# Kernel optimization log

Hardware: AMD Instinct MI355X
Metric: run time of the kernel (lower is better)

Reference implementation:

```python
import jax, jax.numpy as jnp
import numpy as np

N, E = 100000, 600000
IN, H = 164, 128
NH = 4  # attention heads over embed_dim H//4 = 32


def layer_norm(x, g, b, eps=1e-5):
    m = x.mean(-1, keepdims=True)
    v = x.var(-1, keepdims=True)
    return (x - m) * jax.lax.rsqrt(v + eps) * g + b


def gcn_conv(x, W, b, src, dst, n):
    # PyG GCNConv: add self-loops, symmetric D^{-1/2}(A+I)D^{-1/2} normalization.
    deg = jnp.ones((n,), x.dtype).at[dst].add(1.0)  # degree of A+I on target nodes
    dinv = jax.lax.rsqrt(deg)
    xw = x @ W  # [n, out]
    msg = xw[src] * (dinv[src] * dinv[dst])[:, None]  # gather + edge-norm
    agg = jax.ops.segment_sum(msg, dst, num_segments=n)  # scatter-add
    agg = agg + xw * (dinv * dinv)[:, None]  # self-loop term
    return agg + b


def mha_seq1(x, Wq, bq, Wk, bk, Wv, bv, Wo, bo):
    # nn.MultiheadAttention with seq_len==1: softmax over a single key -> weights==1.
    dh = x.shape[-1] // NH
    q = (x @ Wq + bq).reshape(-1, NH, dh)
    k = (x @ Wk + bk).reshape(-1, NH, dh)
    v = (x @ Wv + bv).reshape(-1, NH, dh)
    scores = jnp.sum(q * k, -1, keepdims=True) / jnp.sqrt(jnp.float32(dh))  # [n,NH,1]
    attn = jax.nn.softmax(scores[..., None], axis=-1)[..., 0]  # all ones, kept for fidelity
    out = (attn * v).reshape(-1, NH * dh)
    return out @ Wo + bo


def setup_inputs() -> dict:
    key = jax.random.key(0)
    ks = jax.random.split(key, 16)

    def kaiming(k, i, o):
        return jax.random.normal(k, (i, o), jnp.float32) * (2.0 / i) ** 0.5

    Ha, Hb, Hc = H, H // 2, H // 4  # 128, 64, 32
    return {
        "x": jax.random.normal(ks[0], (N, IN), jnp.float32),
        "edge_index": jax.random.randint(ks[1], (2, E), 0, N),
        "Wi": kaiming(ks[2], IN, Ha), "bi": jnp.zeros((Ha,), jnp.float32),
        "g1": jnp.ones((Ha,), jnp.float32), "b1": jnp.zeros((Ha,), jnp.float32),
        "Wg1": kaiming(ks[3], Ha, Ha), "bg1": jnp.zeros((Ha,), jnp.float32),
        "Wg2": kaiming(ks[4], Ha, Hb), "bg2": jnp.zeros((Hb,), jnp.float32),
        "g2": jnp.ones((Hb,), jnp.float32), "b2": jnp.zeros((Hb,), jnp.float32),
        "Wg3": kaiming(ks[5], Hb, Hc), "bg3": jnp.zeros((Hc,), jnp.float32),
        "Wq": kaiming(ks[6], Hc, Hc), "bq": jnp.zeros((Hc,), jnp.float32),
        "Wk": kaiming(ks[7], Hc, Hc), "bk": jnp.zeros((Hc,), jnp.float32),
        "Wv": kaiming(ks[8], Hc, Hc), "bv": jnp.zeros((Hc,), jnp.float32),
        "Wo": kaiming(ks[9], Hc, Hc), "bo": jnp.zeros((Hc,), jnp.float32),
        "Wc1": kaiming(ks[10], Hc, H // 8), "bc1": jnp.zeros((H // 8,), jnp.float32),
        "Wc2": kaiming(ks[11], H // 8, 32), "bc2": jnp.zeros((32,), jnp.float32),
        "Wc3": kaiming(ks[12], 32, 1), "bc3": jnp.zeros((1,), jnp.float32),
    }


def reference(x, edge_index, Wi, bi, g1, b1, Wg1, bg1, Wg2, bg2, g2, b2,
              Wg3, bg3, Wq, bq, Wk, bk, Wv, bv, Wo, bo,
              Wc1, bc1, Wc2, bc2, Wc3, bc3):
    src, dst = edge_index[0], edge_index[1]
    n = x.shape[0]
    # dropout layers are identity in eval mode
    h = layer_norm(jax.nn.relu(x @ Wi + bi), g1, b1)
    h1 = jax.nn.relu(gcn_conv(h, Wg1, bg1, src, dst, n)) + h
    h2 = layer_norm(jax.nn.relu(gcn_conv(h1, Wg2, bg2, src, dst, n)), g2, b2)
    h3 = jax.nn.relu(gcn_conv(h2, Wg3, bg3, src, dst, n))
    h3 = mha_seq1(h3, Wq, bq, Wk, bk, Wv, bv, Wo, bo)
    h3 = jax.nn.relu(h3 @ Wc1 + bc1)
    h3 = jax.nn.relu(h3 @ Wc2 + bc2)
    return (h3 @ Wc3 + bc3)[:, 0]
```

## Files before the change

### kernel.cpp

```cpp
#include <hip/hip_runtime.h>


typedef __attribute__((ext_vector_type(8))) _Float16 f16x8;
typedef __attribute__((ext_vector_type(4))) _Float16 f16x4;
typedef __attribute__((ext_vector_type(4))) float f32x4;

template <int V> struct IC { static constexpr int value = V; };

#define GLOAD_LDS16(gp, lp)                                        \
  __builtin_amdgcn_global_load_lds(                                \
      (const __attribute__((address_space(1))) void*)(gp),         \
      (__attribute__((address_space(3))) void*)(lp), 16, 0, 0)

template <int NV>
static __device__ __forceinline__ void wait_vm() {
  asm volatile("s_waitcnt vmcnt(%0)" :: "n"(NV) : "memory");
}
static __device__ __forceinline__ void wait_lgkm0() {
  asm volatile("s_waitcnt lgkmcnt(0)" ::: "memory");
  __builtin_amdgcn_sched_barrier(0);
}

__global__ void k_count(const int* __restrict__ dst, int* __restrict__ counts, int e) {
  int i = blockIdx.x * blockDim.x + threadIdx.x;
  if (i < e) atomicAdd(&counts[dst[i]], 1);
}

__global__ __launch_bounds__(256) void k_scan_part(
    const int* __restrict__ counts, int* __restrict__ bsums, int n) {
  int tid = threadIdx.x;
  int i0 = blockIdx.x * 1024 + tid * 4;
  int s = 0;
#pragma unroll
  for (int k = 0; k < 4; k++) { int i = i0 + k; if (i < n) s += counts[i]; }
#pragma unroll
  for (int d = 1; d < 64; d <<= 1) s += __shfl_xor(s, d);
  __shared__ int wsum[4];
  int lane = tid & 63, w = tid >> 6;
  if (lane == 0) wsum[w] = s;
  __syncthreads();
  if (tid == 0) bsums[blockIdx.x] = wsum[0] + wsum[1] + wsum[2] + wsum[3];
}

__global__ __launch_bounds__(256) void k_scan_down(
    int* __restrict__ counts, const int* __restrict__ bsums,
    int* __restrict__ offsets, float* __restrict__ dinv, int n, int e, int nb) {
  int tid = threadIdx.x;
  int lane = tid & 63, w = tid >> 6;
  __shared__ int wsum[4], psum[4];
  int pv = (tid < nb && tid < blockIdx.x) ? bsums[tid] : 0;
#pragma unroll
  for (int d = 1; d < 64; d <<= 1) pv += __shfl_xor(pv, d);
  if (lane == 0) psum[w] = pv;
  __syncthreads();
  int blockpref = psum[0] + psum[1] + psum[2] + psum[3];

  int i0 = blockIdx.x * 1024 + tid * 4;
  int c[4]; int tsum = 0;
#pragma unroll
  for (int k = 0; k < 4; k++) { int i = i0 + k; c[k] = (i < n) ? counts[i] : 0; tsum += c[k]; }
  int v = tsum;
#pragma unroll
  for (int d = 1; d < 64; d <<= 1) { int t = __shfl_up(v, d); if (lane >= d) v += t; }
  if (lane == 63) wsum[w] = v;
  __syncthreads();
  int wadd = 0;
#pragma unroll
  for (int q = 0; q < 4; q++) if (q < w) wadd += wsum[q];
  int run = (v - tsum) + wadd + blockpref;
#pragma unroll
  for (int k = 0; k < 4; k++) {
    int i = i0 + k;
    if (i < n) {
      offsets[i] = run;
      dinv[i] = rsqrtf((float)(c[k] + 1));
      counts[i] = 0;
    }
    run += c[k];
  }
  if (blockIdx.x == 0 && tid == 0) offsets[n] = e;
}

__global__ void k_fill(const int* __restrict__ src, const int* __restrict__ dst,
                       const int* __restrict__ offsets, int* __restrict__ cursor,
                       const float* __restrict__ dinv, int2* __restrict__ csr, int e) {
  int i = blockIdx.x * blockDim.x + threadIdx.x;
  if (i >= e) return;
  int s = src[i], d = dst[i];
  int pos = atomicAdd(&cursor[d], 1);
  csr[offsets[d] + pos] = make_int2(s, __float_as_int(dinv[s] * dinv[d]));
}

__device__ __forceinline__ void pack_hi(const float* __restrict__ W,
                                        _Float16* __restrict__ dst,
                                        int K, int N, int u) {
  int lane = u & 63; int rest = u >> 6; int CT = N >> 4;
  int ct = rest % CT, ks = rest / CT;
  int gcol = ct * 16 + (lane & 15);
  int gk0 = ks * 32 + (lane >> 4) * 8;
  size_t o = (size_t)(ks * CT + ct) * 512 + lane * 8;
#pragma unroll
  for (int i = 0; i < 8; i++) {
    float v = (gk0 + i < K) ? W[(size_t)(gk0 + i) * N + gcol] : 0.0f;
    dst[o + i] = (_Float16)v;
  }
}

__global__ void k_setup(const float* __restrict__ Wi, const float* __restrict__ Wg1,
                        const float* __restrict__ Wg2, const float* __restrict__ Wg3,
                        _Float16* __restrict__ pWi, _Float16* __restrict__ pWg1,
                        _Float16* __restrict__ pWg2, _Float16* __restrict__ pWg3,
                        int* __restrict__ counts, float* __restrict__ zp, int n) {
  int b = blockIdx.x;
  if (b < 25) {
    int t = b * 256 + threadIdx.x;
    if (t < 3072) pack_hi(Wi, pWi, 164, 128, t);
    else if (t < 5120) pack_hi(Wg1, pWg1, 128, 128, t - 3072);
    else if (t < 6144) pack_hi(Wg2, pWg2, 128, 64, t - 5120);
    else if (t < 6400) pack_hi(Wg3, pWg3, 64, 32, t - 6144);
  } else {
    if (b == 25 && threadIdx.x < 64) zp[threadIdx.x] = 0.0f;
    int i = (b - 25) * 256 + threadIdx.x;
    if (i < n) counts[i] = 0;
  }
}

__global__ __launch_bounds__(512, 4) void k_gemm_in(
    const float* __restrict__ x, const _Float16* __restrict__ pB,
    const float* __restrict__ bias, const float* __restrict__ gamma,
    const float* __restrict__ beta, const float* __restrict__ zp,
    _Float16* __restrict__ out, int n) {
  constexpr int N = 128, CT = 8;
  __shared__ __align__(16) float sAi[8][3][512];
  int tid = threadIdx.x;
  int lane = tid & 63, w = tid >> 6;
  int rowbase = blockIdx.x * 128 + w * 16;
  const f16x8* Bf = (const f16x8*)pB;

  auto stage = [&](int ks, int buf) {
#pragma unroll
    for (int j = 0; j < 2; j++) {
      int r_ = j * 8 + (lane >> 3);
      int c_ = (lane & 7) ^ (lane >> 3);
      int rg = rowbase + r_;
      bool ok = (rg < n) && (ks < 5 || c_ == 0);
      const void* s = ok ? (const void*)(x + (size_t)rg * 164 + ks * 32 + c_ * 4)
                         : (const void*)zp;
      GLOAD_LDS16(s, &sAi[w][buf][j * 256]);
    }
  };

  f32x4 acc[CT];
#pragma unroll
  for (int c = 0; c < CT; c++) acc[c] = (f32x4)0.0f;

  int rr = lane & 15;
  int c0 = (lane >> 4) * 2;
  int s0 = c0 ^ (rr & 7);
  int s1 = (c0 + 1) ^ (rr & 7);

  f16x8 bfr[2][CT];
  stage(0, 0);
  stage(1, 1);
#pragma unroll
  for (int c = 0; c < CT; c++) bfr[0][c] = Bf[c * 64 + lane];

  auto step = [&](auto ksc, auto wnc) {
    constexpr int ks = decltype(ksc)::value;
    constexpr int WN = decltype(wnc)::value;
    if constexpr (ks + 1 < 6) {
#pragma unroll
      for (int c = 0; c < CT; c++)
        bfr[(ks + 1) & 1][c] = Bf[((ks + 1) * CT + c) * 64 + lane];
    }
    if constexpr (ks + 2 < 6) stage(ks + 2, (ks + 2) % 3);
    wait_vm<WN>();
    const float* bp = &sAi[w][ks % 3][0];
    float4 u0 = *(const float4*)&bp[rr * 32 + s0 * 4];
    float4 u1 = *(const float4*)&bp[rr * 32 + s1 * 4];
    float v[8] = {u0.x, u0.y, u0.z, u0.w, u1.x, u1.y, u1.z, u1.w};
    f16x8 ah;
#pragma unroll
    for (int i = 0; i < 8; i++) ah[i] = (_Float16)v[i];
#pragma unroll
    for (int c = 0; c < CT; c++)
      acc[c] = __builtin_amdgcn_mfma_f32_16x16x32_f16(ah, bfr[ks & 1][c], acc[c], 0, 0, 0);
  };
  step(IC<0>{}, IC<10>{});
  step(IC<1>{}, IC<12>{});
  step(IC<2>{}, IC<12>{});
  step(IC<3>{}, IC<12>{});
  step(IC<4>{}, IC<10>{});
  step(IC<5>{}, IC<0>{});

  int r0 = (lane >> 4) * 4;
  int li = lane & 15;
  float s1v[4] = {0, 0, 0, 0}, s2v[4] = {0, 0, 0, 0};
#pragma unroll
  for (int c = 0; c < CT; c++) {
    float bb = bias[c * 16 + li];
#pragma unroll
    for (int r = 0; r < 4; r++) {
      float t = acc[c][r] + bb;
      t = t > 0.0f ? t : 0.0f;
      acc[c][r] = t;
      s1v[r] += t;
      s2v[r] += t * t;
    }
  }
#pragma unroll
  for (int m = 1; m < 16; m <<= 1) {
#pragma unroll
    for (int r = 0; r < 4; r++) {
      s1v[r] += __shfl_xor(s1v[r], m);
      s2v[r] += __shfl_xor(s2v[r], m);
    }
  }
  wait_lgkm0();
  _Float16* lr = (_Float16*)&sAi[w][0][0];
#pragma unroll
  for (int c = 0; c < CT; c++) {
    float gv = gamma[c * 16 + li], bv = beta[c * 16 + li];
#pragma unroll
    for (int r = 0; r < 4; r++) {
      float mean = s1v[r] * (1.0f / N);
      float var = s2v[r] * (1.0f / N) - mean * mean;
      float rs = rsqrtf(var + 1e-5f);
      lr[(r0 + r) * 128 + c * 16 + li] =
          (_Float16)((acc[c][r] - mean) * rs * gv + bv);
    }
  }
  wait_lgkm0();
#pragma unroll
  for (int i = 0; i < 4; i++) {
    int chunk = i * 64 + lane;
    int rloc = chunk >> 4;
    int cc = chunk & 15;
    if (rowbase + rloc < n)
      *(f16x8*)&out[(size_t)(rowbase + rloc) * 128 + cc * 8] =
          *(const f16x8*)&lr[chunk * 8];
  }
}

template <int K, int N>
__global__ __launch_bounds__(512, 2) void k_gemm_f16(
    const _Float16* __restrict__ A, const _Float16* __restrict__ pB,
    const float* __restrict__ zp, _Float16* __restrict__ out, int n) {
  constexpr int KS = K / 32, CT = N / 16;
  __shared__ __align__(16) _Float16 sB[KS * CT * 512];
  __shared__ __align__(16) _Float16 sA[8][KS][512];
  int tid = threadIdx.x;
  int lane = tid & 63, w = tid >> 6;
  int rowbase = blockIdx.x * 128 + w * 16;

  for (int u = w; u < KS * CT; u += 8)
    GLOAD_LDS16(pB + (size_t)u * 512 + lane * 8, &sB[(size_t)u * 512]);

  int r_ = lane >> 2;
  int c_ = (lane & 3) ^ ((r_ >> 1) & 3);
  int rg = rowbase + r_;
  bool rok = rg < n;
  for (int ks = 0; ks < KS; ks++) {
    const void* s = rok ? (const void*)(A + (size_t)rg * K + ks * 32 + c_ * 8)
                        : (const void*)zp;
    GLOAD_LDS16(s, &sA[w][ks][0]);
  }
  wait_vm<KS>();
  __builtin_amdgcn_s_barrier();

  f32x4 acc[CT];
#pragma unroll
  for (int c = 0; c < CT; c++) acc[c] = (f32x4)0.0f;

  int rr = lane & 15;
  int slot = (lane >> 4) ^ ((rr >> 1) & 3);

  auto cstep = [&](auto ksc) {
    constexpr int ks = decltype(ksc)::value;
    wait_vm<KS - 1 - ks>();
    f16x8 av = *(const f16x8*)&sA[w][ks][rr * 32 + slot * 8];
#pragma unroll
    for (int c = 0; c < CT; c++) {
      f16x8 b = *(const f16x8*)&sB[(size_t)(ks * CT + c) * 512 + lane * 8];
      acc[c] = __builtin_amdgcn_mfma_f32_16x16x32_f16(av, b, acc[c], 0, 0, 0);
    }
  };
  cstep(IC<0>{});
  if constexpr (KS > 1) cstep(IC<1>{});
  if constexpr (KS > 2) cstep(IC<2>{});
  if constexpr (KS > 3) cstep(IC<3>{});

  int r0 = (lane >> 4) * 4;
  int li = lane & 15;
  wait_lgkm0();
  _Float16* lr = &sA[w][0][0];
#pragma unroll
  for (int c = 0; c < CT; c++) {
#pragma unroll
    for (int r = 0; r < 4; r++)
      lr[(r0 + r) * N + c * 16 + li] = (_Float16)acc[c][r];
  }
  wait_lgkm0();
#pragma unroll
  for (int i = 0; i < N / 32; i++) {
    int chunk = i * 64 + lane;
    int rloc = chunk / (N / 8);
    int cc = chunk % (N / 8);
    if (rowbase + rloc < n)
      *(f16x8*)&out[(size_t)(rowbase + rloc) * N + cc * 8] =
          *(const f16x8*)&lr[chunk * 8];
  }
}

template <int OUT_D, int MODE>
__global__ __launch_bounds__(256, 2) void k_gather8(
    const int* __restrict__ off, const int2* __restrict__ csr,
    const _Float16* __restrict__ xw, const float* __restrict__ dinv,
    const float* __restrict__ bias, const _Float16* __restrict__ auxh,
    const float* __restrict__ gamma, const float* __restrict__ beta,
    _Float16* __restrict__ out, int n) {
  constexpr int TPN = OUT_D / 8;
  constexpr int NPB = 256 / TPN;
  int tid = threadIdx.x;
  int node = blockIdx.x * NPB + tid / TPN;
  int li = tid % TPN;
  if (node >= n) return;
  int start = off[node], end = off[node + 1];
  float di = dinv[node];
  float d2 = di * di;
  const _Float16* xp = xw + 8 * li;
  f16x8 self = *(const f16x8*)(xp + (size_t)node * OUT_D);
  f16x8 hres;
  if constexpr (MODE == 0)
    hres = *(const f16x8*)(auxh + (size_t)node * OUT_D + 8 * li);
  float a[8];
#pragma unroll
  for (int q = 0; q < 8; q++) a[q] = (float)self[q] * d2 + bias[8 * li + q];
  for (int cb = start; cb < end; cb += TPN) {
    int m = end - cb; if (m > TPN) m = TPN;
    int sv = node; float nv = 0.0f;
    if (li < m) { int2 me = csr[cb + li]; sv = me.x; nv = __int_as_float(me.y); }
    for (int j0 = 0; j0 < m; j0 += 8) {
      int s[8]; float wv[8];
#pragma unroll
      for (int q = 0; q < 8; q++) {
        s[q] = __shfl(sv, j0 + q, TPN);
        wv[q] = __shfl(nv, j0 + q, TPN);
      }
      f16x8 v[8];
#pragma unroll
      for (int q = 0; q < 8; q++) v[q] = *(const f16x8*)(xp + (size_t)s[q] * OUT_D);
#pragma unroll
      for (int q = 0; q < 8; q++) {
#pragma unroll
        for (int c = 0; c < 8; c++) a[c] += (float)v[q][c] * wv[q];
      }
    }
  }
  _Float16* po = out + (size_t)node * OUT_D + 8 * li;
  if constexpr (MODE == 0) {
    f16x8 o;
#pragma unroll
    for (int q = 0; q < 8; q++)
      o[q] = (_Float16)((a[q] > 0.0f ? a[q] : 0.0f) + (float)hres[q]);
    *(f16x8*)po = o;
  } else {
    float s1 = 0.0f, s2 = 0.0f;
#pragma unroll
    for (int q = 0; q < 8; q++) {
      a[q] = a[q] > 0.0f ? a[q] : 0.0f;
      s1 += a[q];
      s2 += a[q] * a[q];
    }
#pragma unroll
    for (int d = 1; d < TPN; d <<= 1) {
      s1 += __shfl_xor(s1, d, TPN);
      s2 += __shfl_xor(s2, d, TPN);
    }
    float m_ = s1 * (1.0f / OUT_D);
    float var = s2 * (1.0f / OUT_D) - m_ * m_;
    float rs = rsqrtf(var + 1e-5f);
    f16x8 o;
#pragma unroll
    for (int q = 0; q < 8; q++)
      o[q] = (_Float16)((a[q] - m_) * rs * gamma[8 * li + q] + beta[8 * li + q]);
    *(f16x8*)po = o;
  }
}

__global__ __launch_bounds__(256, 2) void k_gather3(
    const int* __restrict__ off, const int2* __restrict__ csr,
    const _Float16* __restrict__ xw, const float* __restrict__ dinv,
    const float* __restrict__ bias, _Float16* __restrict__ out, int n) {
  constexpr int OUT_D = 32, TPN = 8, NPB = 32;
  int tid = threadIdx.x;
  int node = blockIdx.x * NPB + tid / TPN;
  int li = tid % TPN;
  if (node >= n) return;
  int start = off[node], end = off[node + 1];
  float di = dinv[node];
  float d2 = di * di;
  const _Float16* xp = xw + 4 * li;
  f16x4 self = *(const f16x4*)(xp + (size_t)node * OUT_D);
  float a0 = (float)self[0] * d2 + bias[4 * li + 0];
  float a1 = (float)self[1] * d2 + bias[4 * li + 1];
  float a2 = (float)self[2] * d2 + bias[4 * li + 2];
  float a3 = (float)self[3] * d2 + bias[4 * li + 3];
  for (int cb = start; cb < end; cb += TPN) {
    int m = end - cb; if (m > TPN) m = TPN;
    int sv = node; float nv = 0.0f;
    if (li < m) { int2 me = csr[cb + li]; sv = me.x; nv = __int_as_float(me.y); }
    for (int j0 = 0; j0 < m; j0 += 8) {
      int s[8]; float wv[8];
#pragma unroll
      for (int q = 0; q < 8; q++) {
        s[q] = __shfl(sv, j0 + q, TPN);
        wv[q] = __shfl(nv, j0 + q, TPN);
      }
      f16x4 v[8];
#pragma unroll
      for (int q = 0; q < 8; q++) v[q] = *(const f16x4*)(xp + (size_t)s[q] * OUT_D);
#pragma unroll
      for (int q = 0; q < 8; q++) {
        a0 += (float)v[q][0] * wv[q];
        a1 += (float)v[q][1] * wv[q];
        a2 += (float)v[q][2] * wv[q];
        a3 += (float)v[q][3] * wv[q];
      }
    }
  }
  f16x4 o;
  o[0] = (_Float16)a0; o[1] = (_Float16)a1;
  o[2] = (_Float16)a2; o[3] = (_Float16)a3;
  *(f16x4*)(out + (size_t)node * OUT_D + 4 * li) = o;
}

__global__ __launch_bounds__(256) void k_tail(
    const _Float16* __restrict__ agg3, const float* __restrict__ Wv,
    const float* __restrict__ bv, const float* __restrict__ Wo,
    const float* __restrict__ bo, const float* __restrict__ Wc1,
    const float* __restrict__ bc1, const float* __restrict__ Wc2,
    const float* __restrict__ bc2, const float* __restrict__ Wc3,
    const float* __restrict__ bc3, float* __restrict__ out, int n) {
  __shared__ float sWv[1024], sWo[1024], sWc1[512], sWc2[512];
  __shared__ float sbv[32], sbo[32], sbc2[32], sWc3[32], sbc1[16], sbc3[1];
  int tid = threadIdx.x;
  for (int i = tid; i < 1024; i += 256) { sWv[i] = Wv[i]; sWo[i] = Wo[i]; }
  for (int i = tid; i < 512; i += 256) { sWc1[i] = Wc1[i]; sWc2[i] = Wc2[i]; }
  if (tid < 32) { sbv[tid] = bv[tid]; sbo[tid] = bo[tid];
                  sbc2[tid] = bc2[tid]; sWc3[tid] = Wc3[tid]; }
  if (tid < 16) sbc1[tid] = bc1[tid];
  if (tid == 0) sbc3[0] = bc3[0];
  __syncthreads();
  int node = blockIdx.x * blockDim.x + tid;
  if (node >= n) return;
  float a[32];
  const f16x8* row8 = (const f16x8*)(agg3 + (size_t)node * 32);
#pragma unroll
  for (int q = 0; q < 4; q++) {
    f16x8 t = row8[q];
#pragma unroll
    for (int i = 0; i < 8; i++) {
      float f = (float)t[i];
      a[8 * q + i] = f > 0.0f ? f : 0.0f;
    }
  }
  float v[32];
#pragma unroll
  for (int j = 0; j < 32; j++) v[j] = sbv[j];
  for (int k = 0; k < 32; k++) {
#pragma unroll
    for (int j = 0; j < 32; j++) v[j] += a[k] * sWv[k * 32 + j];
  }
  float o[32];
#pragma unroll
  for (int j = 0; j < 32; j++) o[j] = sbo[j];
  for (int k = 0; k < 32; k++) {
#pragma unroll
    for (int j = 0; j < 32; j++) o[j] += v[k] * sWo[k * 32 + j];
  }
  float c1[16];
#pragma unroll
  for (int j = 0; j < 16; j++) c1[j] = sbc1[j];
  for (int k = 0; k < 32; k++) {
#pragma unroll
    for (int j = 0; j < 16; j++) c1[j] += o[k] * sWc1[k * 16 + j];
  }
#pragma unroll
  for (int j = 0; j < 16; j++) c1[j] = c1[j] > 0.0f ? c1[j] : 0.0f;
  float c2[32];
#pragma unroll
  for (int j = 0; j < 32; j++) c2[j] = sbc2[j];
  for (int k = 0; k < 16; k++) {
#pragma unroll
    for (int j = 0; j < 32; j++) c2[j] += c1[k] * sWc2[k * 32 + j];
  }
  float r = sbc3[0];
#pragma unroll
  for (int k = 0; k < 32; k++) {
    float c = c2[k] > 0.0f ? c2[k] : 0.0f;
    r += c * sWc3[k];
  }
  out[node] = r;
}

extern "C" void kernel_launch(void* const* d_in, const int* in_sizes, int n_in,
                              void* d_out, int out_size, void* d_ws, size_t ws_size,
                              hipStream_t stream) {
  const float* x   = (const float*)d_in[0];
  const int* ei    = (const int*)d_in[1];
  const float* Wi  = (const float*)d_in[2];
  const float* bi  = (const float*)d_in[3];
  const float* g1  = (const float*)d_in[4];
  const float* b1  = (const float*)d_in[5];
  const float* Wg1 = (const float*)d_in[6];
  const float* bg1 = (const float*)d_in[7];
  const float* Wg2 = (const float*)d_in[8];
  const float* bg2 = (const float*)d_in[9];
  const float* g2  = (const float*)d_in[10];
  const float* b2  = (const float*)d_in[11];
  const float* Wg3 = (const float*)d_in[12];
  const float* bg3 = (const float*)d_in[13];
  const float* Wv  = (const float*)d_in[18];
  const float* bv  = (const float*)d_in[19];
  const float* Wo  = (const float*)d_in[20];
  const float* bo  = (const float*)d_in[21];
  const float* Wc1 = (const float*)d_in[22];
  const float* bc1 = (const float*)d_in[23];
  const float* Wc2 = (const float*)d_in[24];
  const float* bc2 = (const float*)d_in[25];
  const float* Wc3 = (const float*)d_in[26];
  const float* bc3 = (const float*)d_in[27];

  const int n = in_sizes[0] / 164;
  const int e = in_sizes[1] / 2;
  const int* src = ei;
  const int* dst = ei + e;

  char* ws = (char*)d_ws;
  size_t off = 0;
  auto alloc = [&](size_t bytes) {
    char* p = ws + off;
    off += (bytes + 255) & ~(size_t)255;
    return p;
  };
  _Float16* A     = (_Float16*)alloc((size_t)n * 128 * 2);
  _Float16* B     = (_Float16*)alloc((size_t)n * 128 * 2);
  _Float16* C     = (_Float16*)alloc((size_t)n * 128 * 2);
  float* dinv     = (float*)alloc((size_t)n * 4);
  int*   counts   = (int*)alloc((size_t)n * 4);
  int*   offsets  = (int*)alloc((size_t)(n + 1) * 4);
  int*   bsums    = (int*)alloc(256 * 4);
  int2*  csr      = (int2*)alloc((size_t)e * 8);
  _Float16* pWi   = (_Float16*)alloc(3072 * 16);
  _Float16* pWg1  = (_Float16*)alloc(2048 * 16);
  _Float16* pWg2  = (_Float16*)alloc(1024 * 16);
  _Float16* pWg3  = (_Float16*)alloc(256 * 16);
  float* zp       = (float*)alloc(64 * 4);
  (void)ws_size;

  const int BS = 256;
  const int SB = (n + 1023) / 1024;
  const int GB = (n + 127) / 128;

  k_setup<<<25 + (n + 255) / 256, 256, 0, stream>>>(
      Wi, Wg1, Wg2, Wg3, pWi, pWg1, pWg2, pWg3, counts, zp, n);

  k_count<<<(e + BS - 1) / BS, BS, 0, stream>>>(dst, counts, e);
  k_scan_part<<<SB, 256, 0, stream>>>(counts, bsums, n);
  k_scan_down<<<SB, 256, 0, stream>>>(counts, bsums, offsets, dinv, n, e, SB);
  k_fill<<<(e + BS - 1) / BS, BS, 0, stream>>>(src, dst, offsets, counts, dinv,
                                               csr, e);

  k_gemm_in<<<GB, 512, 0, stream>>>(x, pWi, bi, g1, b1, zp, A, n);

  k_gemm_f16<128, 128><<<GB, 512, 0, stream>>>(A, pWg1, zp, B, n);
  k_gather8<128, 0><<<(n + 15) / 16, 256, 0, stream>>>(
      offsets, csr, B, dinv, bg1, A, nullptr, nullptr, C, n);

  k_gemm_f16<128, 64><<<GB, 512, 0, stream>>>(C, pWg2, zp, A, n);
  k_gather8<64, 1><<<(n + 31) / 32, 256, 0, stream>>>(
      offsets, csr, A, dinv, bg2, nullptr, g2, b2, B, n);

  k_gemm_f16<64, 32><<<GB, 512, 0, stream>>>(B, pWg3, zp, A, n);
  k_gather3<<<(n + 31) / 32, 256, 0, stream>>>(
      offsets, csr, A, dinv, bg3, C, n);

  k_tail<<<(n + BS - 1) / BS, BS, 0, stream>>>(
      C, Wv, bv, Wo, bo, Wc1, bc1, Wc2, bc2, Wc3, bc3, (float*)d_out, n);
}
```

Measured before the change: 214.2 us.

## Fuse first GCN weight GEMM into input GEMM+layernorm kernel

The input projection kernel now keeps the layer-normed tile in LDS and immediately multiplies it by Wg1, writing both the normalized features and the XW product. This removes a separate GEMM launch and the re-read of the 128-wide fp16 activation from global memory. Launch-bound occupancy hints for the gather kernels are also raised from 2 to 4 blocks, which may force register spilling. Wg1 fragments are loaded directly from global per wave rather than staged in LDS, which adds redundant global traffic.

```diff
diff --git a/kernel.cpp b/kernel.cpp
--- a/kernel.cpp
+++ b/kernel.cpp
@@ -125,17 +125,19 @@
   }
 }
 
-__global__ __launch_bounds__(512, 4) void k_gemm_in(
+__global__ __launch_bounds__(512, 4) void k_gemm_in1(
     const float* __restrict__ x, const _Float16* __restrict__ pB,
-    const float* __restrict__ bias, const float* __restrict__ gamma,
-    const float* __restrict__ beta, const float* __restrict__ zp,
-    _Float16* __restrict__ out, int n) {
+    const _Float16* __restrict__ pB1, const float* __restrict__ bias,
+    const float* __restrict__ gamma, const float* __restrict__ beta,
+    const float* __restrict__ zp, _Float16* __restrict__ outH,
+    _Float16* __restrict__ outXW, int n) {
   constexpr int N = 128, CT = 8;
   __shared__ __align__(16) float sAi[8][3][512];
   int tid = threadIdx.x;
   int lane = tid & 63, w = tid >> 6;
   int rowbase = blockIdx.x * 128 + w * 16;
   const f16x8* Bf = (const f16x8*)pB;
+  const f16x8* Bf1 = (const f16x8*)pB1;
 
   auto stage = [&](int ks, int buf) {
 #pragma unroll
@@ -237,7 +239,39 @@
     int rloc = chunk >> 4;
     int cc = chunk & 15;
     if (rowbase + rloc < n)
-      *(f16x8*)&out[(size_t)(rowbase + rloc) * 128 + cc * 8] =
+      *(f16x8*)&outH[(size_t)(rowbase + rloc) * 128 + cc * 8] =
+          *(const f16x8*)&lr[chunk * 8];
+  }
+
+  int kof = (lane >> 4) * 8;
+#pragma unroll
+  for (int c = 0; c < CT; c++) acc[c] = (f32x4)0.0f;
+#pragma unroll
+  for (int ks = 0; ks < 4; ks++) {
+    f16x8 b1[CT];
+#pragma unroll
+    for (int c = 0; c < CT; c++) b1[c] = Bf1[(ks * CT + c) * 64 + lane];
+    f16x8 av = *(const f16x8*)&lr[rr * 128 + ks * 32 + kof];
+    wait_vm<0>();
+#pragma unroll
+    for (int c = 0; c < CT; c++)
+      acc[c] = __builtin_amdgcn_mfma_f32_16x16x32_f16(av, b1[c], acc[c], 0, 0, 0);
+  }
+  wait_lgkm0();
+#pragma unroll
+  for (int c = 0; c < CT; c++) {
+#pragma unroll
+    for (int r = 0; r < 4; r++)
+      lr[(r0 + r) * 128 + c * 16 + li] = (_Float16)acc[c][r];
+  }
+  wait_lgkm0();
+#pragma unroll
+  for (int i = 0; i < 4; i++) {
+    int chunk = i * 64 + lane;
+    int rloc = chunk >> 4;
+    int cc = chunk & 15;
+    if (rowbase + rloc < n)
+      *(f16x8*)&outXW[(size_t)(rowbase + rloc) * 128 + cc * 8] =
           *(const f16x8*)&lr[chunk * 8];
   }
 }
@@ -313,7 +347,7 @@
 }
 
 template <int OUT_D, int MODE>
-__global__ __launch_bounds__(256, 2) void k_gather8(
+__global__ __launch_bounds__(256, 4) void k_gather8(
     const int* __restrict__ off, const int2* __restrict__ csr,
     const _Float16* __restrict__ xw, const float* __restrict__ dinv,
     const float* __restrict__ bias, const _Float16* __restrict__ auxh,
@@ -388,7 +422,7 @@
   }
 }
 
-__global__ __launch_bounds__(256, 2) void k_gather3(
+__global__ __launch_bounds__(256, 4) void k_gather3(
     const int* __restrict__ off, const int2* __restrict__ csr,
     const _Float16* __restrict__ xw, const float* __restrict__ dinv,
     const float* __restrict__ bias, _Float16* __restrict__ out, int n) {
@@ -572,9 +606,8 @@
   k_fill<<<(e + BS - 1) / BS, BS, 0, stream>>>(src, dst, offsets, counts, dinv,
                                                csr, e);
 
-  k_gemm_in<<<GB, 512, 0, stream>>>(x, pWi, bi, g1, b1, zp, A, n);
-
-  k_gemm_f16<128, 128><<<GB, 512, 0, stream>>>(A, pWg1, zp, B, n);
+  k_gemm_in1<<<GB, 512, 0, stream>>>(x, pWi, pWg1, bi, g1, b1, zp, A, B, n);
+
   k_gather8<128, 0><<<(n + 15) / 16, 256, 0, stream>>>(
       offsets, csr, B, dinv, bg1, A, nullptr, nullptr, C, n);
 
```

Result: no change. 210.7 us (-1.6%).
